# Optimization experiments

Measured on AMD Instinct MI355X. Metric: run time of the kernel, lower is better.

## Reference

```python
import jax, jax.numpy as jnp
import numpy as np

BN_EPS = 1e-3  # keras BatchNormalization default epsilon


def setup_inputs() -> dict:
    key = jax.random.key(0)
    ks = jax.random.split(key, 8)
    B, H, W, C, K, CLS = 8, 64, 64, 512, 32, 21
    std = 1.0 / (K * C) ** 0.5
    x = jax.random.normal(ks[0], (B, H, W, C), dtype=jnp.float32)
    codewords = jax.random.uniform(ks[1], (C, K), dtype=jnp.float32, minval=-std, maxval=std)
    smoothing_factors = jax.random.uniform(ks[2], (K,), dtype=jnp.float32, minval=-1.0, maxval=0.0)
    # BatchNormalization(axis=-2) over (B, features, K): per-feature params, inference stats
    bn_gamma = jnp.ones((C,), dtype=jnp.float32)
    bn_beta = jnp.zeros((C,), dtype=jnp.float32)
    bn_mean = jnp.zeros((C,), dtype=jnp.float32)
    bn_var = jnp.ones((C,), dtype=jnp.float32)
    # Dense layers (glorot-uniform style init)
    lim1 = (6.0 / (C + C)) ** 0.5
    w_enc = jax.random.uniform(ks[3], (C, C), dtype=jnp.float32, minval=-lim1, maxval=lim1)
    b_enc = jnp.zeros((C,), dtype=jnp.float32)
    lim2 = (6.0 / (C + CLS)) ** 0.5
    w_se = jax.random.uniform(ks[4], (C, CLS), dtype=jnp.float32, minval=-lim2, maxval=lim2)
    b_se = jnp.zeros((CLS,), dtype=jnp.float32)
    return {"x": x, "codewords": codewords, "smoothing_factors": smoothing_factors,
            "bn_gamma": bn_gamma, "bn_beta": bn_beta, "bn_mean": bn_mean, "bn_var": bn_var,
            "w_enc": w_enc, "b_enc": b_enc, "w_se": w_se, "b_se": b_se}


def _encoder(x, codewords, smoothing_factors, bn_gamma, bn_beta, bn_mean, bn_var):
    B, H, W, C = x.shape
    K = codewords.shape[1]
    N = H * W
    xf = x.reshape(B, N, C)
    # squared residual norms ||x_n - c_k||^2 via expansion (same math as the
    # explicit (B,N,C,K) residual tensor in the original, without materializing it)
    x_sq = jnp.sum(xf * xf, axis=-1, keepdims=True)          # (B,N,1)
    cw_sq = jnp.sum(codewords * codewords, axis=0)            # (K,)
    cross = jnp.einsum('bnc,ck->bnk', xf, codewords)          # (B,N,K)
    sqnorms = x_sq - 2.0 * cross + cw_sq                      # (B,N,K)
    # softmax over codewords of -(sqnorm * smoothing_factor)
    weights = jax.nn.softmax(-(sqnorms * smoothing_factors), axis=-1)  # (B,N,K)
    # sum_n w_nk * (x_n - c_k) = (w^T x)_ck - c_k * sum_n w_nk
    wx = jnp.einsum('bnk,bnc->bck', weights, xf)              # (B,C,K)
    wsum = jnp.sum(weights, axis=1)                           # (B,K)
    enc = wx - codewords[None, :, :] * wsum[:, None, :]       # (B,C,K)
    # BatchNorm(axis=-2) in inference mode: normalize per-feature across (B,K)
    inv = jax.lax.rsqrt(bn_var + BN_EPS)
    enc_bn = (enc - bn_mean[None, :, None]) * (inv * bn_gamma)[None, :, None] + bn_beta[None, :, None]
    enc_relu = jax.nn.relu(enc_bn)
    out = jnp.sum(enc_relu, axis=-1)                          # (B,C)
    return out.reshape(B, 1, 1, C)


def reference(x, codewords, smoothing_factors, bn_gamma, bn_beta, bn_mean, bn_var,
              w_enc, b_enc, w_se, b_se):
    B = x.shape[0]
    C = codewords.shape[0]
    encodings = _encoder(x, codewords, smoothing_factors, bn_gamma, bn_beta, bn_mean, bn_var)  # (B,1,1,C)
    attn = jax.nn.sigmoid(jnp.einsum('bijc,cd->bijd', encodings, w_enc) + b_enc)  # (B,1,1,C)
    featuremaps_output = attn * x                                                  # (B,H,W,C)
    enc_vec = encodings.reshape(B, C)
    se_loss_output = jax.nn.sigmoid(enc_vec @ w_se + b_se)                         # (B,classes)
    return featuremaps_output, se_loss_output
```

## Files before the change

### kernel.cpp

```cpp
#include <hip/hip_runtime.h>

#define BB 8
#define NN 4096
#define CCH 512
#define KK 32
#define CLS 21
#define BN_EPS 1e-3f

#define CHUNK 128
#define NBLK (NN / CHUNK)

typedef _Float16 f16;
typedef _Float16 f16x8 __attribute__((ext_vector_type(8)));
typedef float f32x4 __attribute__((ext_vector_type(4)));

#define WP 136

#define WS_P    0
#define WS_WSP  (NBLK * BB * CCH * KK)
#define WS_ENC  (WS_WSP + NBLK * BB * KK)
#define WS_END  (WS_ENC + BB * CCH)

template <int CTRL>
__device__ __forceinline__ float dpp_add(float v) {
    int r = __builtin_amdgcn_update_dpp(0, __builtin_bit_cast(int, v),
                                        CTRL, 0xF, 0xF, true);
    return v + __builtin_bit_cast(float, r);
}
template <int CTRL>
__device__ __forceinline__ float dpp_max(float v) {
    int r = __builtin_amdgcn_update_dpp(0, __builtin_bit_cast(int, v),
                                        CTRL, 0xF, 0xF, true);
    return fmaxf(v, __builtin_bit_cast(float, r));
}
__device__ __forceinline__ float rowsum16(float v) {
    v = dpp_add<0x128>(v); v = dpp_add<0x124>(v);
    v = dpp_add<0x122>(v); v = dpp_add<0x121>(v);
    return v;
}
__device__ __forceinline__ float rowmax16(float v) {
    v = dpp_max<0x128>(v); v = dpp_max<0x124>(v);
    v = dpp_max<0x122>(v); v = dpp_max<0x121>(v);
    return v;
}

__global__ __launch_bounds__(512, 2) void enc_mfma(
    const float* __restrict__ x, const float* __restrict__ cw,
    const float* __restrict__ sf, float* __restrict__ ws)
{
    __shared__ f16   cwL[2048 * 8];
    __shared__ f16   wexch[32 * WP];
    __shared__ float wsq[8][KK];
    __shared__ float csqL[KK];
    __shared__ float nsfL[KK];
    __shared__ float redtmp[8][KK];

    const int t = threadIdx.x;
    const int w = t >> 6, l = t & 63, a = l & 15, g = l >> 4;
    const int chunk = blockIdx.x, b = blockIdx.y;
    const int n0 = chunk * CHUNK;

#pragma unroll
    for (int si = 0; si < 4; ++si) {
        const int s     = si * 512 + t;
        const int lane  = s & 63;
        const int cstep = (s >> 6) & 15;
        const int kt    = s >> 10;
        const int k     = (lane & 15) + 16 * kt;
        const int c0    = cstep * 32 + (lane >> 4) * 8;
        f16x8 v;
#pragma unroll
        for (int i = 0; i < 8; ++i) v[i] = (f16)cw[(c0 + i) * KK + k];
        *reinterpret_cast<f16x8*>(cwL + (size_t)s * 8) = v;
    }
    if (t < 256) {
        const int k = t & 31, part = t >> 5;
        float s = 0.f;
        for (int c = part * 64; c < part * 64 + 64; ++c) {
            const float v = cw[c * KK + k];
            s += v * v;
        }
        redtmp[part][k] = s;
    }
    __syncthreads();
    if (t < KK) {
        float s = 0.f;
#pragma unroll
        for (int p = 0; p < 8; ++p) s += redtmp[p][t];
        csqL[t] = s;
        nsfL[t] = -sf[t];
    }
    __syncthreads();

    const float csq0 = csqL[a], csq1 = csqL[a + 16];
    const float nsf0 = nsfL[a], nsf1 = nsfL[a + 16];

    f32x4 d0 = {0.f, 0.f, 0.f, 0.f}, d1 = {0.f, 0.f, 0.f, 0.f};
    float xs = 0.f;
    {
        const float* xrow = x + (size_t)(b * NN + n0 + w * 16 + a) * CCH;
#pragma unroll
        for (int cs = 0; cs < 16; ++cs) {
            const int c0 = cs * 32 + g * 8;
            const float4 u0 = *reinterpret_cast<const float4*>(xrow + c0);
            const float4 u1 = *reinterpret_cast<const float4*>(xrow + c0 + 4);
            xs += u0.x*u0.x + u0.y*u0.y + u0.z*u0.z + u0.w*u0.w
                + u1.x*u1.x + u1.y*u1.y + u1.z*u1.z + u1.w*u1.w;
            const f16x8 af = {(f16)u0.x, (f16)u0.y, (f16)u0.z, (f16)u0.w,
                              (f16)u1.x, (f16)u1.y, (f16)u1.z, (f16)u1.w};
            const f16x8 bf0 = *reinterpret_cast<const f16x8*>(
                cwL + ((size_t)cs * 64 + l) * 8);
            const f16x8 bf1 = *reinterpret_cast<const f16x8*>(
                cwL + ((size_t)(16 + cs) * 64 + l) * 8);
            d0 = __builtin_amdgcn_mfma_f32_16x16x32_f16(af, bf0, d0, 0, 0, 0);
            d1 = __builtin_amdgcn_mfma_f32_16x16x32_f16(af, bf1, d1, 0, 0, 0);
        }
        xs += __shfl_xor(xs, 16);
        xs += __shfl_xor(xs, 32);
    }

    float wsacc0 = 0.f, wsacc1 = 0.f;
#pragma unroll
    for (int r = 0; r < 4; ++r) {
        const int rho = g * 4 + r;
        const float xsr = __shfl(xs, rho);
        const float l0 = (xsr - 2.f * d0[r] + csq0) * nsf0;
        const float l1 = (xsr - 2.f * d1[r] + csq1) * nsf1;
        const float mx = rowmax16(fmaxf(l0, l1));
        const float e0 = __expf(l0 - mx);
        const float e1 = __expf(l1 - mx);
        const float inv = 1.f / rowsum16(e0 + e1);
        const float w0 = e0 * inv, w1 = e1 * inv;
        wsacc0 += w0; wsacc1 += w1;
        wexch[(a     ) * WP + w * 16 + rho] = (f16)w0;
        wexch[(a + 16) * WP + w * 16 + rho] = (f16)w1;
    }
    wsacc0 += __shfl_xor(wsacc0, 16); wsacc0 += __shfl_xor(wsacc0, 32);
    wsacc1 += __shfl_xor(wsacc1, 16); wsacc1 += __shfl_xor(wsacc1, 32);
    if (l < 16) { wsq[w][l] = wsacc0; wsq[w][l + 16] = wsacc1; }

    __syncthreads();

    f32x4 acc[4][2];
#pragma unroll
    for (int ct = 0; ct < 4; ++ct)
#pragma unroll
        for (int kt = 0; kt < 2; ++kt) acc[ct][kt] = (f32x4){0.f, 0.f, 0.f, 0.f};

    const int c0 = w * 64;
#pragma unroll
    for (int sq2 = 0; sq2 < 4; ++sq2) {
        const f16x8 a0 = *reinterpret_cast<const f16x8*>(
            &wexch[(a     ) * WP + sq2 * 32 + g * 8]);
        const f16x8 a1 = *reinterpret_cast<const f16x8*>(
            &wexch[(a + 16) * WP + sq2 * 32 + g * 8]);
        const float* xb = x + (size_t)(b * NN + n0 + sq2 * 32 + g * 8) * CCH;
#pragma unroll
        for (int ct = 0; ct < 4; ++ct) {
            const int c = c0 + ct * 16 + a;
            f16x8 B;
#pragma unroll
            for (int i = 0; i < 8; ++i) B[i] = (f16)xb[(size_t)i * CCH + c];
            acc[ct][0] = __builtin_amdgcn_mfma_f32_16x16x32_f16(a0, B, acc[ct][0], 0, 0, 0);
            acc[ct][1] = __builtin_amdgcn_mfma_f32_16x16x32_f16(a1, B, acc[ct][1], 0, 0, 0);
        }
    }

    {
        float* pp = ws + WS_P + ((size_t)(chunk * BB + b)) * CCH * KK;
#pragma unroll
        for (int ct = 0; ct < 4; ++ct) {
            const int c = c0 + ct * 16 + a;
#pragma unroll
            for (int kt = 0; kt < 2; ++kt)
                *reinterpret_cast<f32x4*>(pp + (size_t)c * KK + kt * 16 + g * 4) = acc[ct][kt];
        }
    }
    if (t < KK) {
        float s = 0.f;
#pragma unroll
        for (int p = 0; p < 8; ++p) s += wsq[p][t];
        ws[WS_WSP + ((size_t)chunk * BB + b) * KK + t] = s;
    }
}

__global__ __launch_bounds__(256) void reduce_encv(
    float* __restrict__ ws, const float* __restrict__ cw,
    const float* __restrict__ gamma, const float* __restrict__ beta,
    const float* __restrict__ mean, const float* __restrict__ var)
{
    __shared__ float wsum_s[KK];
    const int b  = blockIdx.y;
    const int cs = blockIdx.x;
    const int t  = threadIdx.x;

    if (t < KK) {
        float s0 = 0.f, s1 = 0.f;
        for (int ch = 0; ch < NBLK; ch += 2) {
            s0 += ws[WS_WSP + ((size_t)(ch + 0) * BB + b) * KK + t];
            s1 += ws[WS_WSP + ((size_t)(ch + 1) * BB + b) * KK + t];
        }
        wsum_s[t] = s0 + s1;
    }
    __syncthreads();

    const int cl = t >> 3;
    const int c  = cs * 32 + cl;
    const int kq = t & 7;
    const float* p = ws + WS_P + ((size_t)b * CCH + c) * KK + kq * 4;
    const size_t stride = (size_t)BB * CCH * KK;

    f32x4 a0 = {0.f, 0.f, 0.f, 0.f}, a1 = {0.f, 0.f, 0.f, 0.f};
    for (int ch = 0; ch < NBLK; ch += 2) {
        a0 += *reinterpret_cast<const f32x4*>(p + (ch + 0) * stride);
        a1 += *reinterpret_cast<const f32x4*>(p + (ch + 1) * stride);
    }
    const f32x4 aa = a0 + a1;

    const float g  = gamma[c] * rsqrtf(var[c] + BN_EPS);
    const float mu = mean[c];
    const float be = beta[c];
    const float4 cv = *reinterpret_cast<const float4*>(cw + c * KK + kq * 4);
    const float4 sv = *reinterpret_cast<const float4*>(&wsum_s[kq * 4]);
    float s = 0.f;
    s += fmaxf((aa[0] - cv.x * sv.x - mu) * g + be, 0.f);
    s += fmaxf((aa[1] - cv.y * sv.y - mu) * g + be, 0.f);
    s += fmaxf((aa[2] - cv.z * sv.z - mu) * g + be, 0.f);
    s += fmaxf((aa[3] - cv.w * sv.w - mu) * g + be, 0.f);
    s += __shfl_xor(s, 1);
    s += __shfl_xor(s, 2);
    s += __shfl_xor(s, 4);
    if (kq == 0) ws[WS_ENC + (size_t)b * CCH + c] = s;
}

__global__ __launch_bounds__(256) void scale_fused(
    const float* __restrict__ x, const float* __restrict__ enc,
    const float* __restrict__ w_enc, const float* __restrict__ b_enc,
    const float* __restrict__ w_se, const float* __restrict__ b_se,
    float* __restrict__ out)
{
    __shared__ float ev[CCH];
    __shared__ float red[4][64];
    __shared__ float attnL[64];

    const int ns = blockIdx.x;
    const int cc = blockIdx.y;
    const int b  = blockIdx.z;
    const int t  = threadIdx.x;

    if (cc == 8) {
        if (ns != 0) return;
        ev[t]       = enc[(size_t)b * CCH + t];
        ev[t + 256] = enc[(size_t)b * CCH + 256 + t];
        __syncthreads();
        if (t < 8 * CLS) {
            const int j = t >> 3, p = t & 7;
            float a = 0.f;
            for (int c = p; c < CCH; c += 8) a += ev[c] * w_se[c * CLS + j];
            a += __shfl_xor(a, 1);
            a += __shfl_xor(a, 2);
            a += __shfl_xor(a, 4);
            if (p == 0)
                out[(size_t)BB * NN * CCH + b * CLS + j] =
                    1.f / (1.f + __expf(-(a + b_se[j])));
        }
        return;
    }

    ev[t]       = enc[(size_t)b * CCH + t];
    ev[t + 256] = enc[(size_t)b * CCH + 256 + t];
    __syncthreads();

    {
        const int c2 = cc * 64 + (t & 63);
        const int p  = t >> 6;
        float a0 = 0.f, a1 = 0.f, a2 = 0.f, a3 = 0.f;
#pragma unroll
        for (int i = 0; i < 128; i += 4) {
            const int c = p * 128 + i;
            a0 += ev[c + 0] * w_enc[(size_t)(c + 0) * CCH + c2];
            a1 += ev[c + 1] * w_enc[(size_t)(c + 1) * CCH + c2];
            a2 += ev[c + 2] * w_enc[(size_t)(c + 2) * CCH + c2];
            a3 += ev[c + 3] * w_enc[(size_t)(c + 3) * CCH + c2];
        }
        red[p][t & 63] = (a0 + a1) + (a2 + a3);
        __syncthreads();
        if (t < 64) {
            const float v = red[0][t] + red[1][t] + red[2][t] + red[3][t]
                          + b_enc[cc * 64 + t];
            attnL[t] = 1.f / (1.f + __expf(-v));
        }
        __syncthreads();
    }

    const int q   = t & 15;
    const int rr0 = t >> 4;
    const f32x4 av = *reinterpret_cast<const f32x4*>(attnL + q * 4);
#pragma unroll 8
    for (int i = 0; i < 32; ++i) {
        const int r = ns * 512 + i * 16 + rr0;
        const size_t off = ((size_t)(b * NN + r)) * CCH + cc * 64 + q * 4;
        const f32x4 xv = *reinterpret_cast<const f32x4*>(x + off);
        __builtin_nontemporal_store(xv * av, reinterpret_cast<f32x4*>(out + off));
    }
}

extern "C" void kernel_launch(void* const* d_in, const int* in_sizes, int n_in,
                              void* d_out, int out_size, void* d_ws, size_t ws_size,
                              hipStream_t stream)
{
    const float* x     = (const float*)d_in[0];
    const float* cw    = (const float*)d_in[1];
    const float* sf    = (const float*)d_in[2];
    const float* gamma = (const float*)d_in[3];
    const float* beta  = (const float*)d_in[4];
    const float* mean  = (const float*)d_in[5];
    const float* var   = (const float*)d_in[6];
    const float* w_enc = (const float*)d_in[7];
    const float* b_enc = (const float*)d_in[8];
    const float* w_se  = (const float*)d_in[9];
    const float* b_se  = (const float*)d_in[10];
    float* out = (float*)d_out;
    float* ws  = (float*)d_ws;

    enc_mfma<<<dim3(NBLK, BB), 512, 0, stream>>>(x, cw, sf, ws);
    reduce_encv<<<dim3(16, BB), 256, 0, stream>>>(ws, cw, gamma, beta, mean, var);
    scale_fused<<<dim3(8, 9, BB), 256, 0, stream>>>(
        x, ws + WS_ENC, w_enc, b_enc, w_se, b_se, out);
}
```

Measured before the change: 62.83 us.

## Fuse encoder and partial-sum reduction into a cooperative kernel with grid sync

Merges the MFMA encoding kernel and the cross-chunk reduction kernel into one cooperative launch separated by a grid-wide barrier, which removes one kernel launch and the gap between the two. The reduction is spread over the same 256 blocks, with 16 channels per block. The codeword squared norms are now computed from the fp16 copy already staged in LDS rather than re-read from global memory. Launch bounds drop to one block per SM for the fused path, and a two-kernel fallback runs if the cooperative launch fails. The grid barrier and the lower occupancy bound may cost more than the launch they remove.

```diff
diff --git a/kernel.cpp b/kernel.cpp
--- a/kernel.cpp
+++ b/kernel.cpp
@@ -1,4 +1,5 @@
 #include <hip/hip_runtime.h>
+#include <hip/hip_cooperative_groups.h>
 
 #define BB 8
 #define NN 4096
@@ -44,20 +45,21 @@
     return v;
 }
 
-__global__ __launch_bounds__(512, 2) void enc_mfma(
+struct EncLds {
+    f16   cwL[2048 * 8];
+    f16   wexch[32 * WP];
+    float wsq[8][KK];
+    float csqL[KK];
+    float nsfL[KK];
+    float redtmp[16][KK];
+};
+
+__device__ __forceinline__ void enc_body(
     const float* __restrict__ x, const float* __restrict__ cw,
-    const float* __restrict__ sf, float* __restrict__ ws)
-{
-    __shared__ f16   cwL[2048 * 8];
-    __shared__ f16   wexch[32 * WP];
-    __shared__ float wsq[8][KK];
-    __shared__ float csqL[KK];
-    __shared__ float nsfL[KK];
-    __shared__ float redtmp[8][KK];
-
-    const int t = threadIdx.x;
+    const float* __restrict__ sf, float* __restrict__ ws,
+    EncLds& S, int chunk, int b, int t)
+{
     const int w = t >> 6, l = t & 63, a = l & 15, g = l >> 4;
-    const int chunk = blockIdx.x, b = blockIdx.y;
     const int n0 = chunk * CHUNK;
 
 #pragma unroll
@@ -71,29 +73,39 @@
         f16x8 v;
 #pragma unroll
         for (int i = 0; i < 8; ++i) v[i] = (f16)cw[(c0 + i) * KK + k];
-        *reinterpret_cast<f16x8*>(cwL + (size_t)s * 8) = v;
-    }
-    if (t < 256) {
-        const int k = t & 31, part = t >> 5;
+        *reinterpret_cast<f16x8*>(S.cwL + (size_t)s * 8) = v;
+    }
+    __syncthreads();
+
+    {
+        const int k = t & 31, cstep = t >> 5;
+        const int kt = k >> 4, kb = k & 15;
         float s = 0.f;
-        for (int c = part * 64; c < part * 64 + 64; ++c) {
-            const float v = cw[c * KK + k];
-            s += v * v;
-        }
-        redtmp[part][k] = s;
+#pragma unroll
+        for (int l4 = 0; l4 < 4; ++l4) {
+            const int lane = (l4 << 4) | kb;
+            const f16x8 v = *reinterpret_cast<const f16x8*>(
+                S.cwL + ((size_t)(kt * 16 + cstep) * 64 + lane) * 8);
+#pragma unroll
+            for (int i = 0; i < 8; ++i) {
+                const float f = (float)v[i];
+                s += f * f;
+            }
+        }
+        S.redtmp[cstep][k] = s;
     }
     __syncthreads();
     if (t < KK) {
         float s = 0.f;
 #pragma unroll
-        for (int p = 0; p < 8; ++p) s += redtmp[p][t];
-        csqL[t] = s;
-        nsfL[t] = -sf[t];
-    }
-    __syncthreads();
-
-    const float csq0 = csqL[a], csq1 = csqL[a + 16];
-    const float nsf0 = nsfL[a], nsf1 = nsfL[a + 16];
+        for (int p = 0; p < 16; ++p) s += S.redtmp[p][t];
+        S.csqL[t] = s;
+        S.nsfL[t] = -sf[t];
+    }
+    __syncthreads();
+
+    const float csq0 = S.csqL[a], csq1 = S.csqL[a + 16];
+    const float nsf0 = S.nsfL[a], nsf1 = S.nsfL[a + 16];
 
     f32x4 d0 = {0.f, 0.f, 0.f, 0.f}, d1 = {0.f, 0.f, 0.f, 0.f};
     float xs = 0.f;
@@ -109,9 +121,9 @@
             const f16x8 af = {(f16)u0.x, (f16)u0.y, (f16)u0.z, (f16)u0.w,
                               (f16)u1.x, (f16)u1.y, (f16)u1.z, (f16)u1.w};
             const f16x8 bf0 = *reinterpret_cast<const f16x8*>(
-                cwL + ((size_t)cs * 64 + l) * 8);
+                S.cwL + ((size_t)cs * 64 + l) * 8);
             const f16x8 bf1 = *reinterpret_cast<const f16x8*>(
-                cwL + ((size_t)(16 + cs) * 64 + l) * 8);
+                S.cwL + ((size_t)(16 + cs) * 64 + l) * 8);
             d0 = __builtin_amdgcn_mfma_f32_16x16x32_f16(af, bf0, d0, 0, 0, 0);
             d1 = __builtin_amdgcn_mfma_f32_16x16x32_f16(af, bf1, d1, 0, 0, 0);
         }
@@ -132,12 +144,12 @@
         const float inv = 1.f / rowsum16(e0 + e1);
         const float w0 = e0 * inv, w1 = e1 * inv;
         wsacc0 += w0; wsacc1 += w1;
-        wexch[(a     ) * WP + w * 16 + rho] = (f16)w0;
-        wexch[(a + 16) * WP + w * 16 + rho] = (f16)w1;
+        S.wexch[(a     ) * WP + w * 16 + rho] = (f16)w0;
+        S.wexch[(a + 16) * WP + w * 16 + rho] = (f16)w1;
     }
     wsacc0 += __shfl_xor(wsacc0, 16); wsacc0 += __shfl_xor(wsacc0, 32);
     wsacc1 += __shfl_xor(wsacc1, 16); wsacc1 += __shfl_xor(wsacc1, 32);
-    if (l < 16) { wsq[w][l] = wsacc0; wsq[w][l + 16] = wsacc1; }
+    if (l < 16) { S.wsq[w][l] = wsacc0; S.wsq[w][l + 16] = wsacc1; }
 
     __syncthreads();
 
@@ -151,9 +163,9 @@
 #pragma unroll
     for (int sq2 = 0; sq2 < 4; ++sq2) {
         const f16x8 a0 = *reinterpret_cast<const f16x8*>(
-            &wexch[(a     ) * WP + sq2 * 32 + g * 8]);
+            &S.wexch[(a     ) * WP + sq2 * 32 + g * 8]);
         const f16x8 a1 = *reinterpret_cast<const f16x8*>(
-            &wexch[(a + 16) * WP + sq2 * 32 + g * 8]);
+            &S.wexch[(a + 16) * WP + sq2 * 32 + g * 8]);
         const float* xb = x + (size_t)(b * NN + n0 + sq2 * 32 + g * 8) * CCH;
 #pragma unroll
         for (int ct = 0; ct < 4; ++ct) {
@@ -179,21 +191,17 @@
     if (t < KK) {
         float s = 0.f;
 #pragma unroll
-        for (int p = 0; p < 8; ++p) s += wsq[p][t];
+        for (int p = 0; p < 8; ++p) s += S.wsq[p][t];
         ws[WS_WSP + ((size_t)chunk * BB + b) * KK + t] = s;
     }
 }
 
-__global__ __launch_bounds__(256) void reduce_encv(
+__device__ __forceinline__ void reduce_body(
     float* __restrict__ ws, const float* __restrict__ cw,
     const float* __restrict__ gamma, const float* __restrict__ beta,
-    const float* __restrict__ mean, const float* __restrict__ var)
-{
-    __shared__ float wsum_s[KK];
-    const int b  = blockIdx.y;
-    const int cs = blockIdx.x;
-    const int t  = threadIdx.x;
-
+    const float* __restrict__ mean, const float* __restrict__ var,
+    float* wsum_s, int cs, int b, int t)
+{
     if (t < KK) {
         float s0 = 0.f, s1 = 0.f;
         for (int ch = 0; ch < NBLK; ch += 2) {
@@ -204,33 +212,67 @@
     }
     __syncthreads();
 
-    const int cl = t >> 3;
-    const int c  = cs * 32 + cl;
-    const int kq = t & 7;
-    const float* p = ws + WS_P + ((size_t)b * CCH + c) * KK + kq * 4;
-    const size_t stride = (size_t)BB * CCH * KK;
-
-    f32x4 a0 = {0.f, 0.f, 0.f, 0.f}, a1 = {0.f, 0.f, 0.f, 0.f};
-    for (int ch = 0; ch < NBLK; ch += 2) {
-        a0 += *reinterpret_cast<const f32x4*>(p + (ch + 0) * stride);
-        a1 += *reinterpret_cast<const f32x4*>(p + (ch + 1) * stride);
-    }
-    const f32x4 aa = a0 + a1;
-
-    const float g  = gamma[c] * rsqrtf(var[c] + BN_EPS);
-    const float mu = mean[c];
-    const float be = beta[c];
-    const float4 cv = *reinterpret_cast<const float4*>(cw + c * KK + kq * 4);
-    const float4 sv = *reinterpret_cast<const float4*>(&wsum_s[kq * 4]);
-    float s = 0.f;
-    s += fmaxf((aa[0] - cv.x * sv.x - mu) * g + be, 0.f);
-    s += fmaxf((aa[1] - cv.y * sv.y - mu) * g + be, 0.f);
-    s += fmaxf((aa[2] - cv.z * sv.z - mu) * g + be, 0.f);
-    s += fmaxf((aa[3] - cv.w * sv.w - mu) * g + be, 0.f);
-    s += __shfl_xor(s, 1);
-    s += __shfl_xor(s, 2);
-    s += __shfl_xor(s, 4);
-    if (kq == 0) ws[WS_ENC + (size_t)b * CCH + c] = s;
+    if (t < 128) {
+        const int cl = t >> 3;
+        const int c  = cs * 16 + cl;
+        const int kq = t & 7;
+        const float* p = ws + WS_P + ((size_t)b * CCH + c) * KK + kq * 4;
+        const size_t stride = (size_t)BB * CCH * KK;
+
+        f32x4 a0 = {0.f, 0.f, 0.f, 0.f}, a1 = {0.f, 0.f, 0.f, 0.f};
+        for (int ch = 0; ch < NBLK; ch += 2) {
+            a0 += *reinterpret_cast<const f32x4*>(p + (ch + 0) * stride);
+            a1 += *reinterpret_cast<const f32x4*>(p + (ch + 1) * stride);
+        }
+        const f32x4 aa = a0 + a1;
+
+        const float g  = gamma[c] * rsqrtf(var[c] + BN_EPS);
+        const float mu = mean[c];
+        const float be = beta[c];
+        const float4 cv = *reinterpret_cast<const float4*>(cw + c * KK + kq * 4);
+        const float4 sv = *reinterpret_cast<const float4*>(&wsum_s[kq * 4]);
+        float s = 0.f;
+        s += fmaxf((aa[0] - cv.x * sv.x - mu) * g + be, 0.f);
+        s += fmaxf((aa[1] - cv.y * sv.y - mu) * g + be, 0.f);
+        s += fmaxf((aa[2] - cv.z * sv.z - mu) * g + be, 0.f);
+        s += fmaxf((aa[3] - cv.w * sv.w - mu) * g + be, 0.f);
+        s += __shfl_xor(s, 1);
+        s += __shfl_xor(s, 2);
+        s += __shfl_xor(s, 4);
+        if (kq == 0) ws[WS_ENC + (size_t)b * CCH + c] = s;
+    }
+}
+
+__global__ __launch_bounds__(512, 1) void enc_reduce_coop(
+    const float* __restrict__ x, const float* __restrict__ cw,
+    const float* __restrict__ sf, const float* __restrict__ gamma,
+    const float* __restrict__ beta, const float* __restrict__ mean,
+    const float* __restrict__ var, float* __restrict__ ws)
+{
+    __shared__ EncLds S;
+    const int t = threadIdx.x;
+    enc_body(x, cw, sf, ws, S, blockIdx.x, blockIdx.y, t);
+    cooperative_groups::this_grid().sync();
+    reduce_body(ws, cw, gamma, beta, mean, var, S.redtmp[0],
+                blockIdx.x, blockIdx.y, t);
+}
+
+__global__ __launch_bounds__(512, 2) void enc_only(
+    const float* __restrict__ x, const float* __restrict__ cw,
+    const float* __restrict__ sf, float* __restrict__ ws)
+{
+    __shared__ EncLds S;
+    enc_body(x, cw, sf, ws, S, blockIdx.x, blockIdx.y, threadIdx.x);
+}
+
+__global__ __launch_bounds__(512) void reduce_only(
+    float* __restrict__ ws, const float* __restrict__ cw,
+    const float* __restrict__ gamma, const float* __restrict__ beta,
+    const float* __restrict__ mean, const float* __restrict__ var)
+{
+    __shared__ float wsum_s[KK];
+    reduce_body(ws, cw, gamma, beta, mean, var, wsum_s,
+                blockIdx.x, blockIdx.y, threadIdx.x);
 }
 
 __global__ __launch_bounds__(256) void scale_fused(
@@ -323,8 +365,15 @@
     float* out = (float*)d_out;
     float* ws  = (float*)d_ws;
 
-    enc_mfma<<<dim3(NBLK, BB), 512, 0, stream>>>(x, cw, sf, ws);
-    reduce_encv<<<dim3(16, BB), 256, 0, stream>>>(ws, cw, gamma, beta, mean, var);
+    void* args[] = {(void*)&x, (void*)&cw, (void*)&sf, (void*)&gamma,
+                    (void*)&beta, (void*)&mean, (void*)&var, (void*)&ws};
+    hipError_t err = hipLaunchCooperativeKernel(
+        (const void*)enc_reduce_coop, dim3(NBLK, BB), dim3(512), args, 0, stream);
+    if (err != hipSuccess) {
+        enc_only<<<dim3(NBLK, BB), 512, 0, stream>>>(x, cw, sf, ws);
+        reduce_only<<<dim3(32, BB), 512, 0, stream>>>(ws, cw, gamma, beta, mean, var);
+    }
+
     scale_fused<<<dim3(8, 9, BB), 256, 0, stream>>>(
         x, ws + WS_ENC, w_enc, b_enc, w_se, b_se, out);
 }
```

New measurement: 114.8 us. 82.6% more time.
